# Kernel tuning notes

Measured on AMD Instinct MI355X. Metric: run time of the kernel, lower is better.

## Reference

```python
import jax, jax.numpy as jnp
import numpy as np

N_HEADS = 16
HEAD_DIM = 64
D_MODEL = N_HEADS * HEAD_DIM
MASK_NUM = -2.0**32 + 1.0
LN_EPS = 1e-8


def setup_inputs() -> dict:
    key = jax.random.key(0)
    ks = jax.random.split(key, 6)
    B, S = 2, 2048
    queries = jax.random.normal(ks[0], (B, S, D_MODEL), dtype=jnp.float32)
    keys = jax.random.normal(ks[1], (B, S, D_MODEL), dtype=jnp.float32)
    values = jax.random.normal(ks[2], (B, S, D_MODEL), dtype=jnp.float32)
    lim = np.sqrt(6.0 / (D_MODEL + D_MODEL)).astype(np.float32)  # glorot_uniform
    Wq = jax.random.uniform(ks[3], (D_MODEL, D_MODEL), jnp.float32, -lim, lim)
    Wk = jax.random.uniform(ks[4], (D_MODEL, D_MODEL), jnp.float32, -lim, lim)
    Wv = jax.random.uniform(ks[5], (D_MODEL, D_MODEL), jnp.float32, -lim, lim)
    gamma = jnp.ones((D_MODEL,), jnp.float32)
    beta = jnp.zeros((D_MODEL,), jnp.float32)
    return {"queries": queries, "keys": keys, "values": values,
            "Wq": Wq, "Wk": Wk, "Wv": Wv, "gamma": gamma, "beta": beta}


def _split_heads(x):
    # [B, S, H*dh] -> tf.split(axis=2)+concat(axis=0) order: [H*B, S, dh]
    B, S, _ = x.shape
    return x.reshape(B, S, N_HEADS, HEAD_DIM).transpose(2, 0, 1, 3).reshape(N_HEADS * B, S, HEAD_DIM)


def _merge_heads(x, B):
    # [H*B, S, dh] -> [B, S, H*dh]
    S = x.shape[1]
    return x.reshape(N_HEADS, B, S, HEAD_DIM).transpose(1, 2, 0, 3).reshape(B, S, D_MODEL)


def reference(queries, keys, values, Wq, Wk, Wv, gamma, beta):
    B = queries.shape[0]
    q = _split_heads(queries @ Wq)   # [HB, Sq, dh]
    k = _split_heads(keys @ Wk)      # [HB, Sk, dh]
    v = _split_heads(values @ Wv)    # [HB, Sk, dh]

    scores = jnp.einsum('bqd,bkd->bqk', q, k) / jnp.float32(np.sqrt(HEAD_DIM))
    # key padding mask: positions whose projected key is all-zero
    kmask = jnp.sign(jnp.sum(jnp.abs(k), axis=-1))  # [HB, Sk]
    scores = jnp.where(kmask[:, None, :] == 0, jnp.float32(MASK_NUM), scores)
    attn = jax.nn.softmax(scores, axis=-1)
    # query mask: zero out rows whose projected query is all-zero
    qmask = jnp.sign(jnp.sum(jnp.abs(q), axis=-1))  # [HB, Sq]
    attn = attn * qmask[:, :, None]
    att_out = jnp.einsum('bqk,bkd->bqd', attn, v)   # [HB, Sq, dh]
    att_out = _merge_heads(att_out, B)               # [B, Sq, D]

    x = att_out + queries
    mean = jnp.mean(x, axis=-1, keepdims=True)
    var = jnp.mean((x - mean) ** 2, axis=-1, keepdims=True)
    norm = (x - mean) / jnp.sqrt(var + LN_EPS)
    return gamma * norm + beta
```

## Files before the change

kernel.cpp:

```cpp
#include <hip/hip_runtime.h>

#define DM   1024
#define SEQ  2048
#define NH   16
#define HD   64
#define ROWS 4096

typedef unsigned short u16;
typedef unsigned int   u32;
typedef __attribute__((ext_vector_type(8))) __bf16 bf16x8;
typedef __attribute__((ext_vector_type(4))) float  f32x4;
typedef __attribute__((ext_vector_type(16))) float f32x16;

__device__ __forceinline__ u16 f2bf(float f) {
  u32 u = __builtin_bit_cast(u32, f);
  u += 0x7fffu + ((u >> 16) & 1u);
  return (u16)(u >> 16);
}

__device__ __forceinline__ void async16(const void* g, void* lds) {
  __builtin_amdgcn_global_load_lds((const __attribute__((address_space(1))) u32*)g,
                                   (__attribute__((address_space(3))) u32*)lds, 16, 0, 0);
}


__global__ __launch_bounds__(256) void k_cvt_act(const float* __restrict__ q,
                                                 const float* __restrict__ k,
                                                 const float* __restrict__ v,
                                                 u16* __restrict__ dst) {
  const float* src = blockIdx.z == 0 ? q : (blockIdx.z == 1 ? k : v);
  u16* d = dst + (size_t)blockIdx.z * ((size_t)ROWS * DM);
  size_t i = ((size_t)blockIdx.x * 256 + threadIdx.x) * 8;
  float4 a = *(const float4*)(src + i);
  float4 b = *(const float4*)(src + i + 4);
  u32 w0 = (u32)f2bf(a.x) | ((u32)f2bf(a.y) << 16);
  u32 w1 = (u32)f2bf(a.z) | ((u32)f2bf(a.w) << 16);
  u32 w2 = (u32)f2bf(b.x) | ((u32)f2bf(b.y) << 16);
  u32 w3 = (u32)f2bf(b.z) | ((u32)f2bf(b.w) << 16);
  uint4 o4; o4.x = w0; o4.y = w1; o4.z = w2; o4.w = w3;
  *(uint4*)(d + i) = o4;
}

__global__ __launch_bounds__(256) void k_cvt_wt(const float* __restrict__ Wq,
                                                const float* __restrict__ Wk,
                                                const float* __restrict__ Wv,
                                                u16* __restrict__ wt) {
  __shared__ float t[32][33];
  const float* W = blockIdx.z == 0 ? Wq : (blockIdx.z == 1 ? Wk : Wv);
  u16* D = wt + (size_t)blockIdx.z * (DM * DM);
  int bx = blockIdx.x * 32, by = blockIdx.y * 32;
  int x = threadIdx.x, y = threadIdx.y;
  for (int i = 0; i < 32; i += 8) t[y + i][x] = W[(size_t)(by + y + i) * DM + bx + x];
  __syncthreads();
  for (int i = 0; i < 32; i += 8) D[(size_t)(bx + y + i) * DM + by + x] = f2bf(t[x][y + i]);
}


__global__ __launch_bounds__(256) void k_gemm(const u16* __restrict__ Abase,
                                              const u16* __restrict__ Btbase,
                                              u16* __restrict__ Cbase) {
  __shared__ u16 As[128 * 32];
  __shared__ u16 Bs[128 * 32];
  const int z = blockIdx.z;
  const u16* A  = Abase  + (size_t)z * ((size_t)ROWS * DM);
  const u16* Bt = Btbase + (size_t)z * (DM * DM);
  u16* C        = Cbase  + (size_t)z * ((size_t)ROWS * DM);
  const float sc = (z == 0) ? 0.18033688011112043f : 1.0f;
  int tid = threadIdx.x, w = tid >> 6, l = tid & 63;
  int fr = l & 15, fq = l >> 4;
  int bid = blockIdx.y * 8 + blockIdx.x;
  int nb  = (bid & 7) * 32 + (bid >> 3);
  int m0 = (nb >> 3) * 128, n0 = (nb & 7) * 128;
  int wr = (w >> 1) * 64, wc = (w & 1) * 64;
  f32x4 acc[4][4];
  for (int i = 0; i < 4; ++i) for (int j = 0; j < 4; ++j) acc[i][j] = (f32x4){0.f, 0.f, 0.f, 0.f};

  for (int k0 = 0; k0 < DM; k0 += 32) {
    __syncthreads();
    for (int c = 0; c < 2; ++c) {
      int loff = (c * 4 + w) * 1024;
      int eoff = (loff >> 1) + l * 8;
      int row = eoff >> 5;
      int blk = (eoff & 31) >> 3;
      int gblk = blk ^ ((row >> 1) & 3);
      async16(A  + (size_t)(m0 + row) * DM + k0 + (gblk << 3), (char*)As + loff);
      async16(Bt + (size_t)(n0 + row) * DM + k0 + (gblk << 3), (char*)Bs + loff);
    }
    __syncthreads();
    bf16x8 af[4], bf[4];
    for (int i = 0; i < 4; ++i) {
      int row = wr + i * 16 + fr;
      af[i] = *(const bf16x8*)(As + row * 32 + ((fq ^ ((row >> 1) & 3)) << 3));
    }
    for (int j = 0; j < 4; ++j) {
      int row = wc + j * 16 + fr;
      bf[j] = *(const bf16x8*)(Bs + row * 32 + ((fq ^ ((row >> 1) & 3)) << 3));
    }
    for (int i = 0; i < 4; ++i)
      for (int j = 0; j < 4; ++j)
        acc[i][j] = __builtin_amdgcn_mfma_f32_16x16x32_bf16(af[i], bf[j], acc[i][j], 0, 0, 0);
  }
  for (int i = 0; i < 4; ++i)
    for (int j = 0; j < 4; ++j)
      for (int jj = 0; jj < 4; ++jj) {
        int row = m0 + wr + i * 16 + fq * 4 + jj;
        int col = n0 + wc + j * 16 + fr;
        C[(size_t)row * DM + col] = f2bf(acc[i][j][jj] * sc);
      }
}


__global__ __launch_bounds__(256) void k_vt(const u16* __restrict__ vproj,
                                            u16* __restrict__ vt) {
  __shared__ u16 t[64][64];
  int y = blockIdx.y;
  int h = y >> 1, b = y & 1;
  int s0 = blockIdx.x * 64;
  int tid = threadIdx.x;
  for (int c = 0; c < 2; ++c) {
    int rr = c * 32 + (tid >> 3);
    int blk = tid & 7;
    uint4 vv = *(const uint4*)(vproj + (size_t)(b * SEQ + s0 + rr) * DM + h * 64 + blk * 8);
    *(uint4*)(&t[rr][((blk ^ (rr & 7)) * 8)]) = vv;
  }
  __syncthreads();
  for (int c = 0; c < 2; ++c) {
    int d = c * 32 + (tid >> 3);
    int p = tid & 7;
    int hb4 = ((d >> 3) & 1) * 4;
    int lb = (p ^ (d & 7)) * 8;
    u16 tmp[8];
    for (int j = 0; j < 8; ++j) {
      int ss = lb + (j ^ hb4);
      tmp[j] = t[ss][((d >> 3) ^ (ss & 7)) * 8 + (d & 7)];
    }
    *(uint4*)(vt + (size_t)(y * 64 + d) * SEQ + s0 + p * 8) = *(uint4*)tmp;
  }
}


__global__ __launch_bounds__(256, 4) void k_attn(const u16* __restrict__ Qp,
                                                 const u16* __restrict__ Kp,
                                                 const u16* __restrict__ Vt,
                                                 float* __restrict__ att) {
  __shared__ u16 lds[2][8192];
  const int tid = threadIdx.x, w = tid >> 6, l = tid & 63;
  const int lrow = l & 31, h = l >> 5;
  const int qh = w & 1, kh = w >> 1;
  const int g = blockIdx.x;
  const int vy = (g & 7) * 4 + ((g >> 3) & 3);
  const int vx = g >> 5;
  const int head = vy >> 1, b = vy & 1;
  const int hcol = head * 64;
  const int q0w = vx * 64 + qh * 32;

  const u16* qrow = Qp + (size_t)(b * SEQ + q0w + lrow) * DM + hcol + h * 8;
  bf16x8 qb0 = *(const bf16x8*)(qrow);
  bf16x8 qb1 = *(const bf16x8*)(qrow + 16);
  bf16x8 qb2 = *(const bf16x8*)(qrow + 32);
  bf16x8 qb3 = *(const bf16x8*)(qrow + 48);

  const int sw = lrow & 7;
  const int kbase = kh * 4096 + lrow * 128;
  const int B0 = kbase + (((0 + h) ^ sw) << 4);
  const int B1 = kbase + (((2 + h) ^ sw) << 4);
  const int B2 = kbase + (((4 + h) ^ sw) << 4);
  const int B3 = kbase + (((6 + h) ^ sw) << 4);

  const int hh = (h * 8) ^ (((lrow >> 3) & 1) * 8);
  const int vb = 8192 + lrow * 128;
  const int V00 = vb + (((4 * kh + 0) ^ sw) << 4) + hh;
  const int V01 = vb + (((4 * kh + 1) ^ sw) << 4) + hh;
  const int V10 = vb + (((4 * kh + 2) ^ sw) << 4) + hh;
  const int V11 = vb + (((4 * kh + 3) ^ sw) << 4) + hh;

  const int ldo0 = w * 1024, ldo1 = (4 + w) * 1024;
  const int e0 = (ldo0 >> 1) + l * 8, e1 = (ldo1 >> 1) + l * 8;
  const int r0 = e0 >> 6, r1 = e1 >> 6;
  const int kb0 = ((e0 & 63) >> 3) ^ (r0 & 7), kb1 = ((e1 & 63) >> 3) ^ (r1 & 7);
  const u16* kp0 = Kp + (size_t)(b * SEQ + r0) * DM + hcol + kb0 * 8;
  const u16* kp1 = Kp + (size_t)(b * SEQ + r1) * DM + hcol + kb1 * 8;
  const u16* vp0 = Vt + (size_t)(vy * 64 + r0) * SEQ + (e0 & 63);
  const u16* vp1 = Vt + (size_t)(vy * 64 + r1) * SEQ + (e1 & 63);

  f32x16 ot0, ot1;
#pragma unroll
  for (int i = 0; i < 16; ++i) { ot0[i] = 0.f; ot1[i] = 0.f; }
  float lacc = 0.f;

  {
    char* dst = (char*)(&lds[0][0]);
    async16(kp0, dst + ldo0);
    async16(kp1, dst + ldo1);
    async16(vp0, dst + 8192 + ldo0);
    async16(vp1, dst + 8192 + ldo1);
    kp0 += 64 * DM; kp1 += 64 * DM; vp0 += 64; vp1 += 64;
  }
  __syncthreads();

  int cur = 0;
  for (int t = 0; t < SEQ / 64; ++t) {
    if (t != SEQ / 64 - 1) {
      char* dst = (char*)(&lds[cur ^ 1][0]);
      async16(kp0, dst + ldo0);
      async16(kp1, dst + ldo1);
      async16(vp0, dst + 8192 + ldo0);
      async16(vp1, dst + 8192 + ldo1);
      kp0 += 64 * DM; kp1 += 64 * DM; vp0 += 64; vp1 += 64;
    }

    const char* Kb = (const char*)(&lds[cur][0]);
    bf16x8 a0 = *(const bf16x8*)(Kb + B0);
    bf16x8 a1 = *(const bf16x8*)(Kb + B1);
    bf16x8 a2 = *(const bf16x8*)(Kb + B2);
    bf16x8 a3 = *(const bf16x8*)(Kb + B3);
    f32x16 st;
#pragma unroll
    for (int i = 0; i < 16; ++i) st[i] = 0.f;
    __builtin_amdgcn_s_setprio(1);
    st = __builtin_amdgcn_mfma_f32_32x32x16_bf16(a0, qb0, st, 0, 0, 0);
    st = __builtin_amdgcn_mfma_f32_32x32x16_bf16(a1, qb1, st, 0, 0, 0);
    st = __builtin_amdgcn_mfma_f32_32x32x16_bf16(a2, qb2, st, 0, 0, 0);
    st = __builtin_amdgcn_mfma_f32_32x32x16_bf16(a3, qb3, st, 0, 0, 0);
    __builtin_amdgcn_s_setprio(0);

    f32x16 p;
#pragma unroll
    for (int i = 0; i < 16; ++i) p[i] = exp2f(st[i]);
    float s0 = (p[0] + p[1]) + (p[2] + p[3]);
    float s1 = (p[4] + p[5]) + (p[6] + p[7]);
    float s2 = (p[8] + p[9]) + (p[10] + p[11]);
    float s3 = (p[12] + p[13]) + (p[14] + p[15]);
    lacc += (s0 + s1) + (s2 + s3);

    bf16x8 pb0, pb1;
#pragma unroll
    for (int j = 0; j < 8; ++j) {
      pb0[j] = (__bf16)p[j];
      pb1[j] = (__bf16)p[8 + j];
    }

    uint2 x0 = *(const uint2*)(Kb + V00), x1 = *(const uint2*)(Kb + V01);
    uint2 x2 = *(const uint2*)(Kb + V10), x3 = *(const uint2*)(Kb + V11);
    uint2 y0 = *(const uint2*)(Kb + 4096 + V00), y1 = *(const uint2*)(Kb + 4096 + V01);
    uint2 y2 = *(const uint2*)(Kb + 4096 + V10), y3 = *(const uint2*)(Kb + 4096 + V11);
    uint4 u0; u0.x = x0.x; u0.y = x0.y; u0.z = x1.x; u0.w = x1.y;
    uint4 u1; u1.x = x2.x; u1.y = x2.y; u1.z = x3.x; u1.w = x3.y;
    uint4 u2; u2.x = y0.x; u2.y = y0.y; u2.z = y1.x; u2.w = y1.y;
    uint4 u3; u3.x = y2.x; u3.y = y2.y; u3.z = y3.x; u3.w = y3.y;
    bf16x8 vf0 = __builtin_bit_cast(bf16x8, u0);
    bf16x8 vf1 = __builtin_bit_cast(bf16x8, u1);
    bf16x8 vf2 = __builtin_bit_cast(bf16x8, u2);
    bf16x8 vf3 = __builtin_bit_cast(bf16x8, u3);
    __builtin_amdgcn_s_setprio(1);
    ot0 = __builtin_amdgcn_mfma_f32_32x32x16_bf16(vf0, pb0, ot0, 0, 0, 0);
    ot0 = __builtin_amdgcn_mfma_f32_32x32x16_bf16(vf1, pb1, ot0, 0, 0, 0);
    ot1 = __builtin_amdgcn_mfma_f32_32x32x16_bf16(vf2, pb0, ot1, 0, 0, 0);
    ot1 = __builtin_amdgcn_mfma_f32_32x32x16_bf16(vf3, pb1, ot1, 0, 0, 0);
    __builtin_amdgcn_s_setprio(0);

    __syncthreads();
    cur ^= 1;
  }

  lacc += __shfl_xor(lacc, 32);
  float* mrg = (float*)&lds[0][0];
  const int slot = qh * 2176;
  if (kh) {
#pragma unroll
    for (int r = 0; r < 16; ++r) {
      mrg[slot + r * 64 + l] = ot0[r];
      mrg[slot + (16 + r) * 64 + l] = ot1[r];
    }
    mrg[slot + 2048 + l] = lacc;
  }
  __syncthreads();
  if (!kh) {
    float inv = 1.f / (lacc + mrg[slot + 2048 + l]);
    float* orow = att + (size_t)(b * SEQ + q0w + lrow) * DM + hcol + 4 * h;
#pragma unroll
    for (int G = 0; G < 4; ++G) {
      float4 w0;
      w0.x = (ot0[4 * G + 0] + mrg[slot + (4 * G + 0) * 64 + l]) * inv;
      w0.y = (ot0[4 * G + 1] + mrg[slot + (4 * G + 1) * 64 + l]) * inv;
      w0.z = (ot0[4 * G + 2] + mrg[slot + (4 * G + 2) * 64 + l]) * inv;
      w0.w = (ot0[4 * G + 3] + mrg[slot + (4 * G + 3) * 64 + l]) * inv;
      *(float4*)(orow + 8 * G) = w0;
      float4 w1;
      w1.x = (ot1[4 * G + 0] + mrg[slot + (16 + 4 * G + 0) * 64 + l]) * inv;
      w1.y = (ot1[4 * G + 1] + mrg[slot + (16 + 4 * G + 1) * 64 + l]) * inv;
      w1.z = (ot1[4 * G + 2] + mrg[slot + (16 + 4 * G + 2) * 64 + l]) * inv;
      w1.w = (ot1[4 * G + 3] + mrg[slot + (16 + 4 * G + 3) * 64 + l]) * inv;
      *(float4*)(orow + 32 + 8 * G) = w1;
    }
  }
}


__global__ __launch_bounds__(256) void k_ln(const float* __restrict__ att,
                                            const float* __restrict__ qin,
                                            const float* __restrict__ gamma,
                                            const float* __restrict__ beta,
                                            float* __restrict__ out) {
  __shared__ float rsum[4], rsum2[4];
  int row = blockIdx.x, t = threadIdx.x;
  size_t off = (size_t)row * DM + t * 4;
  float4 a = *(const float4*)(att + off);
  float4 q = *(const float4*)(qin + off);
  float4 x; x.x = a.x + q.x; x.y = a.y + q.y; x.z = a.z + q.z; x.w = a.w + q.w;
  float s = x.x + x.y + x.z + x.w;
  float s2 = x.x * x.x + x.y * x.y + x.z * x.z + x.w * x.w;
  for (int o2 = 1; o2 < 64; o2 <<= 1) { s += __shfl_xor(s, o2); s2 += __shfl_xor(s2, o2); }
  int w = t >> 6, l = t & 63;
  if (l == 0) { rsum[w] = s; rsum2[w] = s2; }
  __syncthreads();
  s = rsum[0] + rsum[1] + rsum[2] + rsum[3];
  s2 = rsum2[0] + rsum2[1] + rsum2[2] + rsum2[3];
  float mean = s * (1.f / DM);
  float var = s2 * (1.f / DM) - mean * mean;
  float rstd = rsqrtf(var + 1e-8f);
  float4 g = *(const float4*)(gamma + t * 4);
  float4 be = *(const float4*)(beta + t * 4);
  float4 r;
  r.x = (x.x - mean) * rstd * g.x + be.x;
  r.y = (x.y - mean) * rstd * g.y + be.y;
  r.z = (x.z - mean) * rstd * g.z + be.z;
  r.w = (x.w - mean) * rstd * g.w + be.w;
  *(float4*)(out + off) = r;
}


extern "C" void kernel_launch(void* const* d_in, const int* in_sizes, int n_in,
                              void* d_out, int out_size, void* d_ws, size_t ws_size,
                              hipStream_t stream) {
  (void)in_sizes; (void)n_in; (void)out_size; (void)ws_size;
  const float* q     = (const float*)d_in[0];
  const float* k     = (const float*)d_in[1];
  const float* v     = (const float*)d_in[2];
  const float* Wq    = (const float*)d_in[3];
  const float* Wk    = (const float*)d_in[4];
  const float* Wv    = (const float*)d_in[5];
  const float* gamma = (const float*)d_in[6];
  const float* beta  = (const float*)d_in[7];
  float* out = (float*)d_out;
  char* ws = (char*)d_ws;

  const size_t ACT_B = 3ull * ROWS * DM * 2;
  const size_t WT_B  = 3ull * DM * DM * 2;

  u16* actb  = (u16*)ws;
  u16* wtb   = (u16*)(ws + ACT_B);
  u16* projb = (u16*)(ws + ACT_B + WT_B);
  u16* vt    = (u16*)ws;
  float* att = (float*)(ws + 8ull * 1024 * 1024);

  k_cvt_act<<<dim3(2048, 1, 3), 256, 0, stream>>>(q, k, v, actb);
  k_cvt_wt<<<dim3(32, 32, 3), dim3(32, 8), 0, stream>>>(Wq, Wk, Wv, wtb);
  k_gemm<<<dim3(8, 32, 3), 256, 0, stream>>>(actb, wtb, projb);
  k_vt<<<dim3(SEQ / 64, NH * 2), 256, 0, stream>>>(projb + 2ull * ROWS * DM, vt);
  k_attn<<<1024, 256, 0, stream>>>(projb, projb + (size_t)ROWS * DM, vt, att);
  k_ln<<<ROWS, 256, 0, stream>>>(att, q, gamma, beta, out);
}
```

Before: 126.9 us.

## Permute V transpose layout for 16-byte LDS reads and MFMA row sums

The V-transpose kernel writes keys in a permuted order, so the attention kernel can fetch each V operand with one 16-byte LDS read instead of two 8-byte reads plus repacking. The softmax denominator is now accumulated by extra MFMAs against a ones vector instead of scalar adds and a cross-lane shuffle. The change also uses the raw exp2 intrinsic and recomputes global addresses from the loop index instead of advancing pointers. The extra MFMAs take matrix-core time, and the sum is taken from bf16-rounded probabilities, which changes accuracy slightly.

```diff
diff --git a/kernel.cpp b/kernel.cpp
--- a/kernel.cpp
+++ b/kernel.cpp
@@ -127,11 +127,12 @@
   for (int c = 0; c < 2; ++c) {
     int d = c * 32 + (tid >> 3);
     int p = tid & 7;
-    int hb4 = ((d >> 3) & 1) * 4;
-    int lb = (p ^ (d & 7)) * 8;
+    int B = p ^ (d & 7);
+    int g = B >> 1, half = B & 1;
     u16 tmp[8];
     for (int j = 0; j < 8; ++j) {
-      int ss = lb + (j ^ hb4);
+      int kj = (j < 4) ? (4 * half + j) : (8 + 4 * half + (j - 4));
+      int ss = 16 * g + kj;
       tmp[j] = t[ss][((d >> 3) ^ (ss & 7)) * 8 + (d & 7)];
     }
     *(uint4*)(vt + (size_t)(y * 64 + d) * SEQ + s0 + p * 8) = *(uint4*)tmp;
@@ -167,34 +168,32 @@
   const int B2 = kbase + (((4 + h) ^ sw) << 4);
   const int B3 = kbase + (((6 + h) ^ sw) << 4);
 
-  const int hh = (h * 8) ^ (((lrow >> 3) & 1) * 8);
   const int vb = 8192 + lrow * 128;
-  const int V00 = vb + (((4 * kh + 0) ^ sw) << 4) + hh;
-  const int V01 = vb + (((4 * kh + 1) ^ sw) << 4) + hh;
-  const int V10 = vb + (((4 * kh + 2) ^ sw) << 4) + hh;
-  const int V11 = vb + (((4 * kh + 3) ^ sw) << 4) + hh;
+  const int V0 = vb + (((4 * kh + 0 + h) ^ sw) << 4);
+  const int V1 = vb + (((4 * kh + 2 + h) ^ sw) << 4);
 
   const int ldo0 = w * 1024, ldo1 = (4 + w) * 1024;
   const int e0 = (ldo0 >> 1) + l * 8, e1 = (ldo1 >> 1) + l * 8;
   const int r0 = e0 >> 6, r1 = e1 >> 6;
   const int kb0 = ((e0 & 63) >> 3) ^ (r0 & 7), kb1 = ((e1 & 63) >> 3) ^ (r1 & 7);
-  const u16* kp0 = Kp + (size_t)(b * SEQ + r0) * DM + hcol + kb0 * 8;
-  const u16* kp1 = Kp + (size_t)(b * SEQ + r1) * DM + hcol + kb1 * 8;
-  const u16* vp0 = Vt + (size_t)(vy * 64 + r0) * SEQ + (e0 & 63);
-  const u16* vp1 = Vt + (size_t)(vy * 64 + r1) * SEQ + (e1 & 63);
-
-  f32x16 ot0, ot1;
-#pragma unroll
-  for (int i = 0; i < 16; ++i) { ot0[i] = 0.f; ot1[i] = 0.f; }
-  float lacc = 0.f;
+  const size_t koff0 = (size_t)(b * SEQ + r0) * DM + hcol + kb0 * 8;
+  const size_t koff1 = (size_t)(b * SEQ + r1) * DM + hcol + kb1 * 8;
+  const size_t voff0 = (size_t)(vy * 64 + r0) * SEQ + (e0 & 63);
+  const size_t voff1 = (size_t)(vy * 64 + r1) * SEQ + (e1 & 63);
+
+  const f32x16 kzero = {};
+  u32 one2 = 0x3F803F80u;
+  uint4 ou; ou.x = one2; ou.y = one2; ou.z = one2; ou.w = one2;
+  const bf16x8 onesA = __builtin_bit_cast(bf16x8, ou);
+
+  f32x16 ot0 = {}, ot1 = {}, ssacc = {};
 
   {
     char* dst = (char*)(&lds[0][0]);
-    async16(kp0, dst + ldo0);
-    async16(kp1, dst + ldo1);
-    async16(vp0, dst + 8192 + ldo0);
-    async16(vp1, dst + 8192 + ldo1);
-    kp0 += 64 * DM; kp1 += 64 * DM; vp0 += 64; vp1 += 64;
+    async16(Kp + koff0, dst + ldo0);
+    async16(Kp + koff1, dst + ldo1);
+    async16(Vt + voff0, dst + 8192 + ldo0);
+    async16(Vt + voff1, dst + 8192 + ldo1);
   }
   __syncthreads();
 
@@ -202,11 +201,12 @@
   for (int t = 0; t < SEQ / 64; ++t) {
     if (t != SEQ / 64 - 1) {
       char* dst = (char*)(&lds[cur ^ 1][0]);
-      async16(kp0, dst + ldo0);
-      async16(kp1, dst + ldo1);
-      async16(vp0, dst + 8192 + ldo0);
-      async16(vp1, dst + 8192 + ldo1);
-      kp0 += 64 * DM; kp1 += 64 * DM; vp0 += 64; vp1 += 64;
+      size_t kadv = (size_t)(t + 1) * (64 * DM);
+      size_t vadv = (size_t)(t + 1) * 64;
+      async16(Kp + kadv + koff0, dst + ldo0);
+      async16(Kp + kadv + koff1, dst + ldo1);
+      async16(Vt + vadv + voff0, dst + 8192 + ldo0);
+      async16(Vt + vadv + voff1, dst + 8192 + ldo1);
     }
 
     const char* Kb = (const char*)(&lds[cur][0]);
@@ -214,11 +214,8 @@
     bf16x8 a1 = *(const bf16x8*)(Kb + B1);
     bf16x8 a2 = *(const bf16x8*)(Kb + B2);
     bf16x8 a3 = *(const bf16x8*)(Kb + B3);
-    f32x16 st;
-#pragma unroll
-    for (int i = 0; i < 16; ++i) st[i] = 0.f;
     __builtin_amdgcn_s_setprio(1);
-    st = __builtin_amdgcn_mfma_f32_32x32x16_bf16(a0, qb0, st, 0, 0, 0);
+    f32x16 st = __builtin_amdgcn_mfma_f32_32x32x16_bf16(a0, qb0, kzero, 0, 0, 0);
     st = __builtin_amdgcn_mfma_f32_32x32x16_bf16(a1, qb1, st, 0, 0, 0);
     st = __builtin_amdgcn_mfma_f32_32x32x16_bf16(a2, qb2, st, 0, 0, 0);
     st = __builtin_amdgcn_mfma_f32_32x32x16_bf16(a3, qb3, st, 0, 0, 0);
@@ -226,12 +223,7 @@
 
     f32x16 p;
 #pragma unroll
-    for (int i = 0; i < 16; ++i) p[i] = exp2f(st[i]);
-    float s0 = (p[0] + p[1]) + (p[2] + p[3]);
-    float s1 = (p[4] + p[5]) + (p[6] + p[7]);
-    float s2 = (p[8] + p[9]) + (p[10] + p[11]);
-    float s3 = (p[12] + p[13]) + (p[14] + p[15]);
-    lacc += (s0 + s1) + (s2 + s3);
+    for (int i = 0; i < 16; ++i) p[i] = __builtin_amdgcn_exp2f(st[i]);
 
     bf16x8 pb0, pb1;
 #pragma unroll
@@ -240,30 +232,25 @@
       pb1[j] = (__bf16)p[8 + j];
     }
 
-    uint2 x0 = *(const uint2*)(Kb + V00), x1 = *(const uint2*)(Kb + V01);
-    uint2 x2 = *(const uint2*)(Kb + V10), x3 = *(const uint2*)(Kb + V11);
-    uint2 y0 = *(const uint2*)(Kb + 4096 + V00), y1 = *(const uint2*)(Kb + 4096 + V01);
-    uint2 y2 = *(const uint2*)(Kb + 4096 + V10), y3 = *(const uint2*)(Kb + 4096 + V11);
-    uint4 u0; u0.x = x0.x; u0.y = x0.y; u0.z = x1.x; u0.w = x1.y;
-    uint4 u1; u1.x = x2.x; u1.y = x2.y; u1.z = x3.x; u1.w = x3.y;
-    uint4 u2; u2.x = y0.x; u2.y = y0.y; u2.z = y1.x; u2.w = y1.y;
-    uint4 u3; u3.x = y2.x; u3.y = y2.y; u3.z = y3.x; u3.w = y3.y;
-    bf16x8 vf0 = __builtin_bit_cast(bf16x8, u0);
-    bf16x8 vf1 = __builtin_bit_cast(bf16x8, u1);
-    bf16x8 vf2 = __builtin_bit_cast(bf16x8, u2);
-    bf16x8 vf3 = __builtin_bit_cast(bf16x8, u3);
+    bf16x8 vf0 = *(const bf16x8*)(Kb + V0);
+    bf16x8 vf1 = *(const bf16x8*)(Kb + V1);
+    bf16x8 vf2 = *(const bf16x8*)(Kb + 4096 + V0);
+    bf16x8 vf3 = *(const bf16x8*)(Kb + 4096 + V1);
     __builtin_amdgcn_s_setprio(1);
     ot0 = __builtin_amdgcn_mfma_f32_32x32x16_bf16(vf0, pb0, ot0, 0, 0, 0);
     ot0 = __builtin_amdgcn_mfma_f32_32x32x16_bf16(vf1, pb1, ot0, 0, 0, 0);
     ot1 = __builtin_amdgcn_mfma_f32_32x32x16_bf16(vf2, pb0, ot1, 0, 0, 0);
     ot1 = __builtin_amdgcn_mfma_f32_32x32x16_bf16(vf3, pb1, ot1, 0, 0, 0);
+    ssacc = __builtin_amdgcn_mfma_f32_32x32x16_bf16(onesA, pb0, ssacc, 0, 0, 0);
+    ssacc = __builtin_amdgcn_mfma_f32_32x32x16_bf16(onesA, pb1, ssacc, 0, 0, 0);
     __builtin_amdgcn_s_setprio(0);
 
     __syncthreads();
     cur ^= 1;
   }
 
-  lacc += __shfl_xor(lacc, 32);
+  const float lacc = ssacc[0];
+
   float* mrg = (float*)&lds[0][0];
   const int slot = qh * 2176;
   if (kh) {
```

New measurement: 116.7 us. 1.09x faster.
